# Performance work log

Hardware: AMD Instinct MI355X
Metric: run time of the kernel (lower is better)

## Reference

```python
import jax, jax.numpy as jnp
import numpy as np

N_NODES = 50000
N_EDGES = 800000
N_GRAPHS = 128


def _gcn_conv(x, W, b, src, dst, n_nodes):
    # PyG GCNConv: h = x @ W; add self-loops; symmetric norm; aggregate; + bias
    h = x @ W  # [N, out]
    loop = jnp.arange(n_nodes, dtype=src.dtype)
    src_all = jnp.concatenate([src, loop])  # source (row)
    dst_all = jnp.concatenate([dst, loop])  # target (col)
    ones = jnp.ones(src_all.shape[0], dtype=h.dtype)
    deg = jax.ops.segment_sum(ones, dst_all, num_segments=n_nodes)  # in-degree w/ self loops
    dis = jnp.where(deg > 0, jax.lax.rsqrt(deg), 0.0)
    norm = dis[src_all] * dis[dst_all]  # [E+N]
    msg = norm[:, None] * h[src_all]  # [E+N, out]
    out = jax.ops.segment_sum(msg, dst_all, num_segments=n_nodes)
    return out + b


def setup_inputs() -> dict:
    key = jax.random.key(0)
    ks = jax.random.split(key, 7)
    x = jax.random.normal(ks[0], (N_NODES, 4), dtype=jnp.float32)
    edge_index = jax.random.randint(ks[1], (2, N_EDGES), 0, N_NODES, dtype=jnp.int64)
    batch = jnp.sort(jax.random.randint(ks[2], (N_NODES,), 0, N_GRAPHS, dtype=jnp.int64))
    # Glorot-ish init for the linear weights, zeros for bias (PyG default)
    W1 = jax.random.normal(ks[3], (4, 64), dtype=jnp.float32) * (1.0 / np.sqrt(4))
    b1 = jnp.zeros((64,), dtype=jnp.float32)
    W2 = jax.random.normal(ks[4], (64, 64), dtype=jnp.float32) * (1.0 / np.sqrt(64))
    b2 = jnp.zeros((64,), dtype=jnp.float32)
    return {"x": x, "edge_index": edge_index, "batch": batch, "num_graphs": N_GRAPHS,
            "W1": W1, "b1": b1, "W2": W2, "b2": b2}


def reference(x, edge_index, batch, num_graphs, W1, b1, W2, b2):
    src, dst = edge_index[0], edge_index[1]
    n = x.shape[0]
    h = jax.nn.relu(_gcn_conv(x, W1, b1, src, dst, n))
    h = jax.nn.relu(_gcn_conv(h, W2, b2, src, dst, n))
    # global_mean_pool: segment mean over graph ids
    sums = jax.ops.segment_sum(h, batch, num_segments=num_graphs)  # [G, 64]
    cnts = jax.ops.segment_sum(jnp.ones((n,), dtype=h.dtype), batch, num_segments=num_graphs)
    return sums / jnp.maximum(cnts, 1.0)[:, None]
```

## Files before the change

kernel.cpp:

```cpp
#include <hip/hip_runtime.h>
#include <hip/hip_fp16.h>

#define NG 128
#define CHUNK 4096

__device__ __forceinline__ int wave_iscan(int v, int lane) {
#pragma unroll
  for (int off = 1; off < 64; off <<= 1) {
    int u = __shfl_up(v, off, 64);
    if (lane >= off) v += u;
  }
  return v;
}


__global__ void bsum_kernel(const int* __restrict__ src, int* __restrict__ bsum, int M) {
  __shared__ int wsum[4];
  int tid = threadIdx.x, lane = tid & 63, wid = tid >> 6;
  int i = blockIdx.x * 256 + tid;
  int v = (i < M) ? src[i] : 0;
  int inc = wave_iscan(v, lane);
  if (lane == 63) wsum[wid] = inc;
  __syncthreads();
  if (tid == 0) bsum[blockIdx.x] = wsum[0] + wsum[1] + wsum[2] + wsum[3];
}

__global__ void bscan_kernel(int* __restrict__ bsum, int nb) {
  __shared__ int wsum[16];
  int tid = threadIdx.x, lane = tid & 63, wid = tid >> 6;
  int v = (tid < nb) ? bsum[tid] : 0;
  int inc = wave_iscan(v, lane);
  if (lane == 63) wsum[wid] = inc;
  __syncthreads();
  if (tid == 0) {
    int a = 0;
#pragma unroll
    for (int w = 0; w < 16; ++w) { int t = wsum[w]; wsum[w] = a; a += t; }
  }
  __syncthreads();
  if (tid < nb) bsum[tid] = inc - v + wsum[wid];
}

__global__ void offadd_kernel(int* __restrict__ off, const int* __restrict__ bsum, int M) {
  __shared__ int wsum[4];
  int tid = threadIdx.x, lane = tid & 63, wid = tid >> 6;
  int i = blockIdx.x * 256 + tid;
  int v = (i < M) ? off[i] : 0;
  int inc = wave_iscan(v, lane);
  if (lane == 63) wsum[wid] = inc;
  __syncthreads();
  if (tid == 0) {
    int a = bsum[blockIdx.x];
#pragma unroll
    for (int w = 0; w < 4; ++w) { int t = wsum[w]; wsum[w] = a; a += t; }
  }
  __syncthreads();
  if (i < M) off[i] = inc - v + wsum[wid];
}


__global__ void hist_kernel(const int* __restrict__ ei, int E, int nblkE, int K,
                            int* __restrict__ off) {
  __shared__ int lh[256];
  int tid = threadIdx.x, blk = blockIdx.x;
  lh[tid] = 0;
  __syncthreads();
  int e0 = blk * CHUNK;
  for (int i = tid; i < CHUNK; i += 256) {
    int e = e0 + i;
    if (e < E) atomicAdd(&lh[ei[E + e] >> 8], 1);
  }
  __syncthreads();
  if (tid < K) off[tid * nblkE + blk] = lh[tid];
}

__global__ void part_kernel(const int* __restrict__ ei, int E, int nblkE, int K,
                            const int* __restrict__ off, unsigned int* __restrict__ epack) {
  __shared__ int lcur[256];
  int tid = threadIdx.x, blk = blockIdx.x;
  if (tid < K) lcur[tid] = off[tid * nblkE + blk];
  __syncthreads();
  int e0 = blk * CHUNK;
  for (int i = tid; i < CHUNK; i += 256) {
    int e = e0 + i;
    if (e < E) {
      unsigned int s = (unsigned int)ei[e], d = (unsigned int)ei[E + e];
      int pos = atomicAdd(&lcur[d >> 8], 1);
      epack[pos] = (s << 8) | (d & 255u);
    }
  }
}

__global__ void csr2_kernel(const int* __restrict__ off, int nblkE, int K,
                            const unsigned int* __restrict__ epack,
                            const float* __restrict__ x, int* __restrict__ deg,
                            int* __restrict__ rowptr, float* __restrict__ dis,
                            float* __restrict__ xs, unsigned short* __restrict__ esrc,
                            int N, int E) {
  __shared__ int lcnt[256];
  __shared__ int lcur[256];
  __shared__ int wsum[4];
  int tid = threadIdx.x, b = blockIdx.x;
  int lane = tid & 63, wid = tid >> 6;
  lcnt[tid] = 0;
  __syncthreads();
  int be0 = off[b * nblkE];
  int be1 = (b + 1 < K) ? off[(b + 1) * nblkE] : E;
  for (int i = be0 + tid; i < be1; i += 256) atomicAdd(&lcnt[epack[i] & 255u], 1);
  __syncthreads();
  int v = lcnt[tid];
  int inc = wave_iscan(v, lane);
  if (lane == 63) wsum[wid] = inc;
  __syncthreads();
  if (tid == 0) {
    int a = be0;
#pragma unroll
    for (int w = 0; w < 4; ++w) { int t = wsum[w]; wsum[w] = a; a += t; }
  }
  __syncthreads();
  int exc = inc - v + wsum[wid];
  lcur[tid] = exc;
  int node = (b << 8) + tid;
  if (node < N) {
    rowptr[node] = exc;
    deg[node] = v;
    float di = rsqrtf((float)v + 1.0f);
    dis[node] = di;
    float4 xv = ((const float4*)x)[node];
    ((float4*)xs)[node] = make_float4(di * xv.x, di * xv.y, di * xv.z, di * xv.w);
  }
  __syncthreads();
  for (int i = be0 + tid; i < be1; i += 256) {
    unsigned int pk = epack[i];
    int pos = atomicAdd(&lcur[pk & 255u], 1);
    esrc[pos] = (unsigned short)(pk >> 8);
  }
}

__global__ void l1_kernel(const int* __restrict__ rowptr, const int* __restrict__ deg,
                          const unsigned short* __restrict__ esrc, const float* __restrict__ xs,
                          const float* __restrict__ x, const float* __restrict__ dis,
                          const float* __restrict__ W1, const float* __restrict__ b1,
                          __half* __restrict__ h1p, int N) {
  int tid = threadIdx.x;
  int lane = tid & 63, wid = tid >> 6;
  int d = __builtin_amdgcn_readfirstlane(blockIdx.x * 4 + wid);
  if (d >= N) return;
  float di = dis[d];
  int p = __builtin_amdgcn_readfirstlane(rowptr[d]);
  int n = __builtin_amdgcn_readfirstlane(deg[d]);
  float a0 = 0.f, a1 = 0.f, a2 = 0.f, a3 = 0.f;
  for (int k = lane; k < n; k += 64) {
    int e = esrc[p + k];
    float4 v = ((const float4*)xs)[e];
    a0 += v.x; a1 += v.y; a2 += v.z; a3 += v.w;
  }
  if (lane == 0) {
    float4 xv = ((const float4*)x)[d];
    a0 = fmaf(di, xv.x, a0); a1 = fmaf(di, xv.y, a1);
    a2 = fmaf(di, xv.z, a2); a3 = fmaf(di, xv.w, a3);
  }
#pragma unroll
  for (int off = 1; off < 64; off <<= 1) {
    a0 += __shfl_xor(a0, off, 64);
    a1 += __shfl_xor(a1, off, 64);
    a2 += __shfl_xor(a2, off, 64);
    a3 += __shfl_xor(a3, off, 64);
  }
  a0 *= di; a1 *= di; a2 *= di; a3 *= di;
  float o = b1[lane] + a0 * W1[lane] + a1 * W1[64 + lane] + a2 * W1[128 + lane] + a3 * W1[192 + lane];
  h1p[(size_t)d * 64 + lane] = __float2half(di * fmaxf(o, 0.0f));
}

__global__ void __launch_bounds__(256)
l2_kernel(const int* __restrict__ rowptr, const int* __restrict__ deg,
          const unsigned short* __restrict__ esrc, const __half* __restrict__ h1p,
          const float* __restrict__ dis, const float* __restrict__ W2,
          const float* __restrict__ b2, const int* __restrict__ batch,
          float* __restrict__ gsum, int N) {
  __shared__ __align__(16) unsigned short ebuf[4][64];
  __shared__ float vbuf[4][64];
  __shared__ float obuf[4][64];
  __shared__ int gbuf[4];
  int tid = threadIdx.x;
  int lane = tid & 63, wid = tid >> 6;
  int d0 = blockIdx.x * 4 + wid;
  bool valid = d0 < N;
  int d = __builtin_amdgcn_readfirstlane(valid ? d0 : N - 1);
  float di = dis[d];
  float acc0 = __half2float(h1p[(size_t)d * 64 + lane]);
  float acc1 = 0.f, acc2 = 0.f, acc3 = 0.f;
  float acc4 = 0.f, acc5 = 0.f, acc6 = 0.f, acc7 = 0.f;
  int p = __builtin_amdgcn_readfirstlane(rowptr[d]);
  int n = __builtin_amdgcn_readfirstlane(deg[d]);
  for (int base = 0; base < n; base += 64) {
    int m64 = n - base;
    if (m64 > 64) m64 = 64;
    ebuf[wid][lane] = esrc[p + base + ((lane < m64) ? lane : (m64 - 1))];
    for (int k = 0; k < m64; k += 16) {
      uint4 wA = *(const uint4*)&ebuf[wid][k];
      uint4 wB = *(const uint4*)&ebuf[wid][k + 8];
      unsigned int ua0 = wA.x, ua1 = wA.y, ua2 = wA.z, ua3 = wA.w;
      unsigned int ub0 = wB.x, ub1 = wB.y, ub2 = wB.z, ub3 = wB.w;
#pragma unroll
      for (int i = 0; i < 8; ++i) {
        unsigned int u = (i == 0) ? ua0 : (i == 1) ? ua1 : (i == 2) ? ua2 : (i == 3) ? ua3
                       : (i == 4) ? ub0 : (i == 5) ? ub1 : (i == 6) ? ub2 : ub3;
        int ea = (int)(u & 0xffffu), eb = (int)(u >> 16);
        float ma = (k + 2 * i < m64) ? 1.0f : 0.0f;
        float mb = (k + 2 * i + 1 < m64) ? 1.0f : 0.0f;
        float va = __half2float(h1p[(size_t)ea * 64 + lane]);
        float vb = __half2float(h1p[(size_t)eb * 64 + lane]);
        switch (i & 3) {
          case 0: acc0 = fmaf(ma, va, acc0); acc1 = fmaf(mb, vb, acc1); break;
          case 1: acc2 = fmaf(ma, va, acc2); acc3 = fmaf(mb, vb, acc3); break;
          case 2: acc4 = fmaf(ma, va, acc4); acc5 = fmaf(mb, vb, acc5); break;
          case 3: acc6 = fmaf(ma, va, acc6); acc7 = fmaf(mb, vb, acc7); break;
        }
      }
    }
  }
  float v = di * (((acc0 + acc1) + (acc2 + acc3)) + ((acc4 + acc5) + (acc6 + acc7)));
  vbuf[wid][lane] = v;
  float o = b2[lane];
  const float4* vb4 = (const float4*)vbuf[wid];
#pragma unroll
  for (int kk = 0; kk < 16; ++kk) {
    float4 vv = vb4[kk];
    o = fmaf(vv.x, W2[(kk * 4 + 0) * 64 + lane], o);
    o = fmaf(vv.y, W2[(kk * 4 + 1) * 64 + lane], o);
    o = fmaf(vv.z, W2[(kk * 4 + 2) * 64 + lane], o);
    o = fmaf(vv.w, W2[(kk * 4 + 3) * 64 + lane], o);
  }
  obuf[wid][lane] = fmaxf(o, 0.0f);
  if (lane == 0) gbuf[wid] = valid ? batch[d] : -1;
  __syncthreads();
  if (wid == 0) {
    float s = 0.0f;
    int cur = gbuf[0];
#pragma unroll
    for (int r = 0; r < 4; ++r) {
      int g = gbuf[r];
      if (g != cur) {
        if (cur >= 0) atomicAdd(&gsum[cur * 64 + lane], s);
        s = 0.0f;
        cur = g;
      }
      if (g >= 0) s += obuf[r][lane];
    }
    if (cur >= 0) atomicAdd(&gsum[cur * 64 + lane], s);
  }
}


__device__ __forceinline__ int lbound(const int* __restrict__ a, int n, int v) {
  int lo = 0, hi = n;
  while (lo < hi) {
    int mid = (lo + hi) >> 1;
    if (a[mid] < v) lo = mid + 1; else hi = mid;
  }
  return lo;
}

__global__ void out_kernel(const float* __restrict__ gsum, const int* __restrict__ batch,
                           int N, float* __restrict__ out) {
  int t = blockIdx.x * blockDim.x + threadIdx.x;
  if (t >= NG * 64) return;
  int g = t >> 6;
  int cnt = lbound(batch, N, g + 1) - lbound(batch, N, g);
  out[t] = gsum[t] / fmaxf((float)cnt, 1.0f);
}


extern "C" void kernel_launch(void* const* d_in, const int* in_sizes, int n_in,
                              void* d_out, int out_size, void* d_ws, size_t ws_size,
                              hipStream_t stream) {
  const float* x = (const float*)d_in[0];
  const int* ei = (const int*)d_in[1];
  const int* batch = (const int*)d_in[2];
  const float* W1 = (const float*)d_in[4];
  const float* b1 = (const float*)d_in[5];
  const float* W2 = (const float*)d_in[6];
  const float* b2 = (const float*)d_in[7];

  const int N = in_sizes[0] / 4;
  const int E = in_sizes[1] / 2;
  const int K = (N + 255) >> 8;
  const int nblkE = (E + CHUNK - 1) / CHUNK;
  const int M2 = K * nblkE;
  const int NB2 = (M2 + 255) / 256;

  float* gsum = (float*)d_ws;
  int* deg = (int*)(gsum + 64 * NG);
  int* rowptr = deg + N;
  float* xs = (float*)(rowptr + N);
  float* dis = xs + (size_t)4 * N;
  __half* h1p = (__half*)(dis + N);
  unsigned short* esrc = (unsigned short*)(dis + N + (size_t)32 * N);
  int* off = (int*)(esrc + E);
  int* bsum2 = off + M2;
  unsigned int* epack = (unsigned int*)(bsum2 + 1024);

  hipMemsetAsync(d_ws, 0, (size_t)64 * NG * 4, stream);

  const int B = 256;
  hist_kernel<<<nblkE, 256, 0, stream>>>(ei, E, nblkE, K, off);
  bsum_kernel<<<NB2, 256, 0, stream>>>(off, bsum2, M2);
  bscan_kernel<<<1, 1024, 0, stream>>>(bsum2, NB2);
  offadd_kernel<<<NB2, 256, 0, stream>>>(off, bsum2, M2);
  part_kernel<<<nblkE, 256, 0, stream>>>(ei, E, nblkE, K, off, epack);
  csr2_kernel<<<K, 256, 0, stream>>>(off, nblkE, K, epack, x, deg, rowptr, dis, xs, esrc, N, E);
  l1_kernel<<<(N + 3) / 4, 256, 0, stream>>>(rowptr, deg, esrc, xs, x, dis, W1, b1, h1p, N);
  l2_kernel<<<(N + 3) / 4, 256, 0, stream>>>(rowptr, deg, esrc, h1p, dis, W2, b2, batch, gsum, N);
  out_kernel<<<(NG * 64 + B - 1) / B, B, 0, stream>>>(gsum, batch, N, (float*)d_out);
}
```

Baseline: 110.8 us.

## Replace per-block offset scan with global bucket atomics in CSR build

The CSR build used to write a per-block, per-bucket offset matrix and scan it with three kernels. It now accumulates bucket counts with global atomics, scans those counts in one small kernel, and reserves each block's ranges with atomicAdd on bucket cursors. A shared-memory staging buffer lets the partition pass count and then scatter locally. The change also shrinks buckets to 128 nodes and halves CHUNK, which gives more buckets and blocks, and it adds occupancy hints to l1/l2. In exchange, the order of edges within a bucket is no longer deterministic, so float sums in aggregation can differ run to run. The packing also assumes node ids fit in 16 bits.

```diff
diff --git a/kernel.cpp b/kernel.cpp
--- a/kernel.cpp
+++ b/kernel.cpp
@@ -2,7 +2,9 @@
 #include <hip/hip_fp16.h>
 
 #define NG 128
-#define CHUNK 4096
+#define CHUNK 2048
+#define BSH 7
+#define BSZ 128
 
 __device__ __forceinline__ int wave_iscan(int v, int lane) {
 #pragma unroll
@@ -13,135 +15,134 @@
   return v;
 }
 
-
-__global__ void bsum_kernel(const int* __restrict__ src, int* __restrict__ bsum, int M) {
-  __shared__ int wsum[4];
-  int tid = threadIdx.x, lane = tid & 63, wid = tid >> 6;
-  int i = blockIdx.x * 256 + tid;
-  int v = (i < M) ? src[i] : 0;
-  int inc = wave_iscan(v, lane);
-  if (lane == 63) wsum[wid] = inc;
-  __syncthreads();
-  if (tid == 0) bsum[blockIdx.x] = wsum[0] + wsum[1] + wsum[2] + wsum[3];
-}
-
-__global__ void bscan_kernel(int* __restrict__ bsum, int nb) {
-  __shared__ int wsum[16];
-  int tid = threadIdx.x, lane = tid & 63, wid = tid >> 6;
-  int v = (tid < nb) ? bsum[tid] : 0;
-  int inc = wave_iscan(v, lane);
-  if (lane == 63) wsum[wid] = inc;
-  __syncthreads();
-  if (tid == 0) {
-    int a = 0;
-#pragma unroll
-    for (int w = 0; w < 16; ++w) { int t = wsum[w]; wsum[w] = a; a += t; }
-  }
-  __syncthreads();
-  if (tid < nb) bsum[tid] = inc - v + wsum[wid];
-}
-
-__global__ void offadd_kernel(int* __restrict__ off, const int* __restrict__ bsum, int M) {
-  __shared__ int wsum[4];
-  int tid = threadIdx.x, lane = tid & 63, wid = tid >> 6;
-  int i = blockIdx.x * 256 + tid;
-  int v = (i < M) ? off[i] : 0;
-  int inc = wave_iscan(v, lane);
-  if (lane == 63) wsum[wid] = inc;
-  __syncthreads();
-  if (tid == 0) {
-    int a = bsum[blockIdx.x];
-#pragma unroll
-    for (int w = 0; w < 4; ++w) { int t = wsum[w]; wsum[w] = a; a += t; }
-  }
-  __syncthreads();
-  if (i < M) off[i] = inc - v + wsum[wid];
-}
-
-
-__global__ void hist_kernel(const int* __restrict__ ei, int E, int nblkE, int K,
-                            int* __restrict__ off) {
-  __shared__ int lh[256];
+__global__ void hist2_kernel(const int* __restrict__ ei, int E, int K,
+                             int* __restrict__ gcnt) {
+  __shared__ int lh[512];
   int tid = threadIdx.x, blk = blockIdx.x;
-  lh[tid] = 0;
+  lh[tid] = 0; lh[tid + 256] = 0;
   __syncthreads();
   int e0 = blk * CHUNK;
   for (int i = tid; i < CHUNK; i += 256) {
     int e = e0 + i;
-    if (e < E) atomicAdd(&lh[ei[E + e] >> 8], 1);
-  }
-  __syncthreads();
-  if (tid < K) off[tid * nblkE + blk] = lh[tid];
-}
-
-__global__ void part_kernel(const int* __restrict__ ei, int E, int nblkE, int K,
-                            const int* __restrict__ off, unsigned int* __restrict__ epack) {
-  __shared__ int lcur[256];
+    if (e < E) atomicAdd(&lh[ei[E + e] >> BSH], 1);
+  }
+  __syncthreads();
+  for (int q = tid; q < K; q += 256) {
+    int c = lh[q];
+    if (c) atomicAdd(&gcnt[q], c);
+  }
+}
+
+__global__ void scanK_kernel(const int* __restrict__ gcnt, int* __restrict__ bbase,
+                             int* __restrict__ bcur, int K) {
+  __shared__ int wsum[8];
+  int tid = threadIdx.x;
+  int lane = tid & 63, wid = tid >> 6;
+  int v = (tid < K) ? gcnt[tid] : 0;
+  int inc = wave_iscan(v, lane);
+  if (lane == 63) wsum[wid] = inc;
+  __syncthreads();
+  if (tid == 0) {
+    int a = 0;
+#pragma unroll
+    for (int w = 0; w < 8; ++w) { int t = wsum[w]; wsum[w] = a; a += t; }
+  }
+  __syncthreads();
+  if (tid < K) {
+    int exc = inc - v + wsum[wid];
+    bbase[tid] = exc;
+    bcur[tid] = exc;
+  }
+}
+
+__global__ void part2_kernel(const int* __restrict__ ei, int E, int K,
+                             int* __restrict__ bcur, unsigned int* __restrict__ epack) {
+  __shared__ int lh[512];
+  __shared__ unsigned int stag[CHUNK];
   int tid = threadIdx.x, blk = blockIdx.x;
-  if (tid < K) lcur[tid] = off[tid * nblkE + blk];
+  lh[tid] = 0; lh[tid + 256] = 0;
   __syncthreads();
   int e0 = blk * CHUNK;
   for (int i = tid; i < CHUNK; i += 256) {
     int e = e0 + i;
     if (e < E) {
       unsigned int s = (unsigned int)ei[e], d = (unsigned int)ei[E + e];
-      int pos = atomicAdd(&lcur[d >> 8], 1);
-      epack[pos] = (s << 8) | (d & 255u);
-    }
-  }
-}
-
-__global__ void csr2_kernel(const int* __restrict__ off, int nblkE, int K,
+      stag[i] = (s << 16) | d;
+      atomicAdd(&lh[d >> BSH], 1);
+    } else {
+      stag[i] = 0xffffffffu;
+    }
+  }
+  __syncthreads();
+  for (int q = tid; q < K; q += 256) {
+    int c = lh[q];
+    lh[q] = c ? atomicAdd(&bcur[q], c) : 0;
+  }
+  __syncthreads();
+  for (int i = tid; i < CHUNK; i += 256) {
+    unsigned int u = stag[i];
+    if (u != 0xffffffffu) {
+      unsigned int s = u >> 16, d = u & 0xffffu;
+      int pos = atomicAdd(&lh[d >> BSH], 1);
+      epack[pos] = (s << BSH) | (d & (BSZ - 1u));
+    }
+  }
+}
+
+__global__ void csr2_kernel(const int* __restrict__ bbase, const int* __restrict__ gcnt,
                             const unsigned int* __restrict__ epack,
                             const float* __restrict__ x, int* __restrict__ deg,
                             int* __restrict__ rowptr, float* __restrict__ dis,
                             float* __restrict__ xs, unsigned short* __restrict__ esrc,
-                            int N, int E) {
-  __shared__ int lcnt[256];
-  __shared__ int lcur[256];
-  __shared__ int wsum[4];
+                            int N, int K) {
+  __shared__ int lcnt[BSZ];
+  __shared__ int lcur[BSZ];
+  __shared__ int wsum[2];
   int tid = threadIdx.x, b = blockIdx.x;
   int lane = tid & 63, wid = tid >> 6;
-  lcnt[tid] = 0;
-  __syncthreads();
-  int be0 = off[b * nblkE];
-  int be1 = (b + 1 < K) ? off[(b + 1) * nblkE] : E;
-  for (int i = be0 + tid; i < be1; i += 256) atomicAdd(&lcnt[epack[i] & 255u], 1);
-  __syncthreads();
-  int v = lcnt[tid];
+  if (tid < BSZ) lcnt[tid] = 0;
+  __syncthreads();
+  int be0 = bbase[b];
+  int be1 = be0 + gcnt[b];
+  for (int i = be0 + tid; i < be1; i += 256) atomicAdd(&lcnt[epack[i] & (BSZ - 1u)], 1);
+  __syncthreads();
+  int v = (tid < BSZ) ? lcnt[tid] : 0;
   int inc = wave_iscan(v, lane);
-  if (lane == 63) wsum[wid] = inc;
+  if (lane == 63 && wid < 2) wsum[wid] = inc;
   __syncthreads();
   if (tid == 0) {
     int a = be0;
 #pragma unroll
-    for (int w = 0; w < 4; ++w) { int t = wsum[w]; wsum[w] = a; a += t; }
-  }
-  __syncthreads();
-  int exc = inc - v + wsum[wid];
-  lcur[tid] = exc;
-  int node = (b << 8) + tid;
-  if (node < N) {
-    rowptr[node] = exc;
-    deg[node] = v;
-    float di = rsqrtf((float)v + 1.0f);
-    dis[node] = di;
-    float4 xv = ((const float4*)x)[node];
-    ((float4*)xs)[node] = make_float4(di * xv.x, di * xv.y, di * xv.z, di * xv.w);
+    for (int w = 0; w < 2; ++w) { int t = wsum[w]; wsum[w] = a; a += t; }
+  }
+  __syncthreads();
+  if (tid < BSZ) {
+    int exc = inc - v + wsum[wid];
+    lcur[tid] = exc;
+    int node = (b << BSH) + tid;
+    if (node < N) {
+      rowptr[node] = exc;
+      deg[node] = v;
+      float di = rsqrtf((float)v + 1.0f);
+      dis[node] = di;
+      float4 xv = ((const float4*)x)[node];
+      ((float4*)xs)[node] = make_float4(di * xv.x, di * xv.y, di * xv.z, di * xv.w);
+    }
   }
   __syncthreads();
   for (int i = be0 + tid; i < be1; i += 256) {
     unsigned int pk = epack[i];
-    int pos = atomicAdd(&lcur[pk & 255u], 1);
-    esrc[pos] = (unsigned short)(pk >> 8);
-  }
-}
-
-__global__ void l1_kernel(const int* __restrict__ rowptr, const int* __restrict__ deg,
-                          const unsigned short* __restrict__ esrc, const float* __restrict__ xs,
-                          const float* __restrict__ x, const float* __restrict__ dis,
-                          const float* __restrict__ W1, const float* __restrict__ b1,
-                          __half* __restrict__ h1p, int N) {
+    int pos = atomicAdd(&lcur[pk & (BSZ - 1u)], 1);
+    esrc[pos] = (unsigned short)(pk >> BSH);
+  }
+}
+
+__global__ void __launch_bounds__(256, 8)
+l1_kernel(const int* __restrict__ rowptr, const int* __restrict__ deg,
+          const unsigned short* __restrict__ esrc, const float* __restrict__ xs,
+          const float* __restrict__ x, const float* __restrict__ dis,
+          const float* __restrict__ W1, const float* __restrict__ b1,
+          __half* __restrict__ h1p, int N) {
   int tid = threadIdx.x;
   int lane = tid & 63, wid = tid >> 6;
   int d = __builtin_amdgcn_readfirstlane(blockIdx.x * 4 + wid);
@@ -172,7 +173,7 @@
   h1p[(size_t)d * 64 + lane] = __float2half(di * fmaxf(o, 0.0f));
 }
 
-__global__ void __launch_bounds__(256)
+__global__ void __launch_bounds__(256, 8)
 l2_kernel(const int* __restrict__ rowptr, const int* __restrict__ deg,
           const unsigned short* __restrict__ esrc, const __half* __restrict__ h1p,
           const float* __restrict__ dis, const float* __restrict__ W2,
@@ -285,31 +286,28 @@
 
   const int N = in_sizes[0] / 4;
   const int E = in_sizes[1] / 2;
-  const int K = (N + 255) >> 8;
+  const int K = (N + BSZ - 1) >> BSH;
   const int nblkE = (E + CHUNK - 1) / CHUNK;
-  const int M2 = K * nblkE;
-  const int NB2 = (M2 + 255) / 256;
 
   float* gsum = (float*)d_ws;
-  int* deg = (int*)(gsum + 64 * NG);
+  int* gcnt = (int*)(gsum + 64 * NG);
+  int* deg = gcnt + 512;
   int* rowptr = deg + N;
   float* xs = (float*)(rowptr + N);
   float* dis = xs + (size_t)4 * N;
   __half* h1p = (__half*)(dis + N);
   unsigned short* esrc = (unsigned short*)(dis + N + (size_t)32 * N);
-  int* off = (int*)(esrc + E);
-  int* bsum2 = off + M2;
-  unsigned int* epack = (unsigned int*)(bsum2 + 1024);
-
-  hipMemsetAsync(d_ws, 0, (size_t)64 * NG * 4, stream);
+  int* bbase = (int*)(esrc + E);
+  int* bcur = bbase + 512;
+  unsigned int* epack = (unsigned int*)(bcur + 512);
+
+  hipMemsetAsync(d_ws, 0, (size_t)(64 * NG + 512) * 4, stream);
 
   const int B = 256;
-  hist_kernel<<<nblkE, 256, 0, stream>>>(ei, E, nblkE, K, off);
-  bsum_kernel<<<NB2, 256, 0, stream>>>(off, bsum2, M2);
-  bscan_kernel<<<1, 1024, 0, stream>>>(bsum2, NB2);
-  offadd_kernel<<<NB2, 256, 0, stream>>>(off, bsum2, M2);
-  part_kernel<<<nblkE, 256, 0, stream>>>(ei, E, nblkE, K, off, epack);
-  csr2_kernel<<<K, 256, 0, stream>>>(off, nblkE, K, epack, x, deg, rowptr, dis, xs, esrc, N, E);
+  hist2_kernel<<<nblkE, 256, 0, stream>>>(ei, E, K, gcnt);
+  scanK_kernel<<<1, 512, 0, stream>>>(gcnt, bbase, bcur, K);
+  part2_kernel<<<nblkE, 256, 0, stream>>>(ei, E, K, bcur, epack);
+  csr2_kernel<<<K, 256, 0, stream>>>(bbase, gcnt, epack, x, deg, rowptr, dis, xs, esrc, N, K);
   l1_kernel<<<(N + 3) / 4, 256, 0, stream>>>(rowptr, deg, esrc, xs, x, dis, W1, b1, h1p, N);
   l2_kernel<<<(N + 3) / 4, 256, 0, stream>>>(rowptr, deg, esrc, h1p, dis, W2, b2, batch, gsum, N);
   out_kernel<<<(NG * 64 + B - 1) / B, B, 0, stream>>>(gsum, batch, N, (float*)d_out);
```

After: 115.3 us. 4.0% more time.
